# Performance work log

Hardware: AMD Instinct MI355X
Metric: run time of the kernel (lower is better)

The kernel has to match this reference:

```python
import jax, jax.numpy as jnp
import numpy as np

B, T, D, C = 8, 4096, 768, 2048

def setup_inputs() -> dict:
    key = jax.random.key(0)
    k1, k2 = jax.random.split(key)
    embed = jax.random.normal(k1, (B, T, D), dtype=jnp.float32)
    cluster_centers = jax.random.normal(k2, (C, D), dtype=jnp.float32)
    return {"embed": embed, "cluster_centers": cluster_centers}

def reference(embed, cluster_centers):
    x_sq = jnp.sum(embed * embed, axis=-1, keepdims=True)          # (b, t, 1)
    c_sq = jnp.sum(cluster_centers * cluster_centers, axis=-1)     # (c,)
    cross = jnp.einsum('btd,cd->btc', embed, cluster_centers)      # (b, t, c)
    sq_dists = x_sq + c_sq[None, None, :] - 2.0 * cross
    dists = jnp.sqrt(jnp.maximum(sq_dists, 0.0))
    # dists argmax of -cdist == argmin of cdist
    clusters = jnp.argmin(dists, axis=-1)                          # (b, t) int
    return clusters
```

## Files before the change

### kernel.cpp

```cpp
#include <hip/hip_runtime.h>

typedef __fp16 f16x2 __attribute__((ext_vector_type(2)));
typedef __fp16 f16x8 __attribute__((ext_vector_type(8)));
typedef float f32x4 __attribute__((ext_vector_type(4)));

constexpr int MM = 32768;
constexpr int NN = 2048;
constexpr int KK = 768;
constexpr int BM = 128;
constexpr int BN = 128;
constexpr int NKT = KK / 32;
constexpr int NA_UNITS = (MM / 16) * NKT;
constexpr int NB_UNITS = (NN / 16) * NKT;

constexpr size_t WS_APACK = 0;
constexpr size_t WS_BPACK = WS_APACK + (size_t)MM * KK * 4;
constexpr size_t WS_CSQ   = WS_BPACK + (size_t)NN * KK * 4;
constexpr size_t WS_SLOT  = WS_CSQ + (size_t)NN * 4;
constexpr size_t WS_NEED  = WS_SLOT + (size_t)MM * 16 * 8;

__device__ __forceinline__ unsigned bc(f16x2 h) {
    return __builtin_bit_cast(unsigned, h);
}


__global__ __launch_bounds__(256)
void fragpack_kernel(const float* __restrict__ A, const float* __restrict__ Bc,
                     uint4* __restrict__ Ap, uint4* __restrict__ Bp) {
    const int task = blockIdx.x * 4 + (threadIdx.x >> 6);
    const int lane = threadIdx.x & 63;
    const int ln15 = lane & 15;
    const int quad = lane >> 4;

    const bool isB = task >= NA_UNITS;
    const int t = isB ? task - NA_UNITS : task;
    const int tile = t / NKT, kt = t % NKT;
    const float* src = (isB ? Bc : A) + (size_t)(tile * 16 + ln15) * KK + kt * 32 + quad * 8;
    uint4* dst = (isB ? Bp : Ap) + (size_t)t * 128 + lane;

    const float4 v0 = *(const float4*)(src);
    const float4 v1 = *(const float4*)(src + 4);
    f16x2 h0 = __builtin_amdgcn_cvt_pkrtz(v0.x, v0.y);
    f16x2 h1 = __builtin_amdgcn_cvt_pkrtz(v0.z, v0.w);
    f16x2 h2 = __builtin_amdgcn_cvt_pkrtz(v1.x, v1.y);
    f16x2 h3 = __builtin_amdgcn_cvt_pkrtz(v1.z, v1.w);
    f16x2 l0 = __builtin_amdgcn_cvt_pkrtz(v0.x-(float)h0[0], v0.y-(float)h0[1]);
    f16x2 l1 = __builtin_amdgcn_cvt_pkrtz(v0.z-(float)h1[0], v0.w-(float)h1[1]);
    f16x2 l2 = __builtin_amdgcn_cvt_pkrtz(v1.x-(float)h2[0], v1.y-(float)h2[1]);
    f16x2 l3 = __builtin_amdgcn_cvt_pkrtz(v1.z-(float)h3[0], v1.w-(float)h3[1]);
    uint4 hv = {bc(h0), bc(h1), bc(h2), bc(h3)};
    uint4 lv = {bc(l0), bc(l1), bc(l2), bc(l3)};
    dst[0]  = hv;
    dst[64] = lv;
}

__global__ __launch_bounds__(64)
void csq_kernel(const float* __restrict__ cc, float* __restrict__ csq) {
    const int cl = blockIdx.x;
    const int lane = threadIdx.x;
    const float4* row = reinterpret_cast<const float4*>(cc + (size_t)cl * KK);
    float s = 0.f;
#pragma unroll
    for (int w = 0; w < KK / (4 * 64); ++w) {
        float4 v = row[w * 64 + lane];
        s = fmaf(v.x, v.x, s); s = fmaf(v.y, v.y, s);
        s = fmaf(v.z, v.z, s); s = fmaf(v.w, v.w, s);
    }
#pragma unroll
    for (int off = 32; off > 0; off >>= 1) s += __shfl_xor(s, off, 64);
    if (lane == 0) csq[cl] = s;
}

#define MF(a, b, c) __builtin_amdgcn_mfma_f32_16x16x32_f16( \
    __builtin_bit_cast(f16x8, a), __builtin_bit_cast(f16x8, b), c, 0, 0, 0)

__global__ __launch_bounds__(256, 2)
void gemm_pack_kernel(const uint4* __restrict__ Ap, const uint4* __restrict__ Bp,
                      const float* __restrict__ csq, uint2* __restrict__ slots) {
    const int gx = blockIdx.x;
    const int gy = blockIdx.y;
    const int tid  = threadIdx.x;
    const int lane = tid & 63;
    const int ln15 = lane & 15;
    const int quad = lane >> 4;
    const int wave = tid >> 6;
    const int wm = wave >> 1, wn = wave & 1;
    const int tbase = gy * BM;
    const int cb    = gx * BN;

    const uint4* a_ptr[4];
    const uint4* b_ptr[4];
#pragma unroll
    for (int i = 0; i < 4; ++i) {
        a_ptr[i] = Ap + (size_t)(gy * 8 + wm * 4 + i) * NKT * 128 + lane;
        b_ptr[i] = Bp + (size_t)(gx * 8 + wn * 4 + i) * NKT * 128 + lane;
    }

    f32x4 acc[4][4];
#pragma unroll
    for (int i = 0; i < 4; ++i)
#pragma unroll
        for (int j = 0; j < 4; ++j) { f32x4 z = {0.f,0.f,0.f,0.f}; acc[i][j] = z; }

    uint4 Ah0[4], Al0[4], Bh0[4], Bl0[4];
    uint4 Ah1[4], Al1[4], Bh1[4], Bl1[4];

    auto load0 = [&](int kt) {
        const int o = kt * 128;
#pragma unroll
        for (int i = 0; i < 4; ++i) {
            Ah0[i] = a_ptr[i][o]; Al0[i] = a_ptr[i][o + 64];
            Bh0[i] = b_ptr[i][o]; Bl0[i] = b_ptr[i][o + 64];
        }
    };
    auto load1 = [&](int kt) {
        const int o = kt * 128;
#pragma unroll
        for (int i = 0; i < 4; ++i) {
            Ah1[i] = a_ptr[i][o]; Al1[i] = a_ptr[i][o + 64];
            Bh1[i] = b_ptr[i][o]; Bl1[i] = b_ptr[i][o + 64];
        }
    };
    auto comp0 = [&]() {
#pragma unroll
        for (int i = 0; i < 4; ++i)
#pragma unroll
            for (int j = 0; j < 4; ++j) {
                acc[i][j] = MF(Ah0[i], Bh0[j], acc[i][j]);
                acc[i][j] = MF(Ah0[i], Bl0[j], acc[i][j]);
                acc[i][j] = MF(Al0[i], Bh0[j], acc[i][j]);
            }
    };
    auto comp1 = [&]() {
#pragma unroll
        for (int i = 0; i < 4; ++i)
#pragma unroll
            for (int j = 0; j < 4; ++j) {
                acc[i][j] = MF(Ah1[i], Bh1[j], acc[i][j]);
                acc[i][j] = MF(Ah1[i], Bl1[j], acc[i][j]);
                acc[i][j] = MF(Al1[i], Bh1[j], acc[i][j]);
            }
    };

    load0(0);
#pragma unroll 1
    for (int kt = 0; kt < NKT; kt += 2) {
        load1(kt + 1);
        comp0();
        if (kt + 2 < NKT) load0(kt + 2);
        comp1();
    }

    float csq4[4];
#pragma unroll
    for (int j = 0; j < 4; ++j) csq4[j] = csq[cb + wn * 64 + j * 16 + ln15];

    float bval[16]; int bidx[16];
#pragma unroll
    for (int i = 0; i < 4; ++i)
#pragma unroll
        for (int r = 0; r < 4; ++r) {
            const int rid = i * 4 + r;
            float bv_ = csq4[0] - 2.0f * acc[i][0][r];
            int   bi_ = cb + wn * 64 + ln15;
#pragma unroll
            for (int j = 1; j < 4; ++j) {
                const float s = csq4[j] - 2.0f * acc[i][j][r];
                const int   c = cb + wn * 64 + j * 16 + ln15;
                if (s < bv_) { bv_ = s; bi_ = c; }
            }
            bval[rid] = bv_; bidx[rid] = bi_;
        }
#pragma unroll
    for (int off = 1; off < 16; off <<= 1) {
#pragma unroll
        for (int rid = 0; rid < 16; ++rid) {
            const float ov = __shfl_xor(bval[rid], off, 64);
            const int   oi = __shfl_xor(bidx[rid], off, 64);
            if (ov < bval[rid] || (ov == bval[rid] && oi < bidx[rid])) {
                bval[rid] = ov; bidx[rid] = oi;
            }
        }
    }

    __shared__ float vtab[256];
    __shared__ int   itab[256];
    if (ln15 == 0) {
#pragma unroll
        for (int i = 0; i < 4; ++i)
#pragma unroll
            for (int r = 0; r < 4; ++r) {
                const int row = wm * 64 + i * 16 + quad * 4 + r;
                vtab[row * 2 + wn] = bval[i * 4 + r];
                itab[row * 2 + wn] = bidx[i * 4 + r];
            }
    }
    __syncthreads();
    if (tid < 128) {
        float v0 = vtab[tid * 2]; int i0 = itab[tid * 2];
        const float v1 = vtab[tid * 2 + 1]; const int i1 = itab[tid * 2 + 1];
        if (v1 < v0 || (v1 == v0 && i1 < i0)) { v0 = v1; i0 = i1; }
        uint2 e; e.x = __float_as_uint(v0); e.y = (unsigned)i0;
        slots[(size_t)(tbase + tid) * 16 + gx] = e;
    }
}

__global__ __launch_bounds__(256)
void slot_reduce_kernel(const uint2* __restrict__ slots, int* __restrict__ out) {
    const int t = blockIdx.x * 256 + threadIdx.x;
    const uint2* s = slots + (size_t)t * 16;
    float bv = __uint_as_float(s[0].x); int bi = (int)s[0].y;
#pragma unroll
    for (int j = 1; j < 16; ++j) {
        const uint2 e = s[j];
        const float v = __uint_as_float(e.x);
        if (v < bv || (v == bv && (int)e.y < bi)) { bv = v; bi = (int)e.y; }
    }
    out[t] = bi;
}


__global__ __launch_bounds__(256)
void init_ws_kernel(unsigned long long* __restrict__ w) {
    w[blockIdx.x * 256 + threadIdx.x] = 0xFFFFFFFFFFFFFFFFull;
}

__global__ __launch_bounds__(256, 2)
void argmin_mfma_kernel(const float* __restrict__ A, const float* __restrict__ Bc,
                        const float* __restrict__ csq,
                        unsigned long long* __restrict__ ws64) {
    __shared__ unsigned lds[4 * 128 * 20];
    constexpr int AH = 0, AL = 2560, BH = 5120;

    const int tid  = threadIdx.x;
    const int lane = tid & 63;
    const int ln15 = lane & 15;
    const int quad = lane >> 4;
    const int wave = tid >> 6;
    const int wm = wave >> 1, wn = wave & 1;
    const int tbase = blockIdx.x * BM;
    const int cb    = blockIdx.y * BN;

    const int sr  = tid >> 1;
    const int skh = tid & 1;
    const float* gA = A  + (size_t)(tbase + sr) * KK + skh * 16;
    const float* gB = Bc + (size_t)(cb   + sr) * KK + skh * 16;
    const int wword = sr * 20 + skh * 8;

    f32x4 acc[4][4];
#pragma unroll
    for (int i = 0; i < 4; ++i)
#pragma unroll
        for (int j = 0; j < 4; ++j) { f32x4 z = {0.f,0.f,0.f,0.f}; acc[i][j] = z; }

    float4 av[4], bv[4];
#pragma unroll
    for (int p = 0; p < 4; ++p) {
        av[p] = *(const float4*)(gA + p * 4);
        bv[p] = *(const float4*)(gB + p * 4);
    }

    int aw[4], bw[4];
#pragma unroll
    for (int i = 0; i < 4; ++i) {
        aw[i] = AH + (wm * 64 + i * 16 + ln15) * 20 + quad * 4;
        bw[i] = BH + (wn * 64 + i * 16 + ln15) * 20 + quad * 4;
    }

    for (int k0 = 0; k0 < KK; k0 += 32) {
        __syncthreads();
#pragma unroll
        for (int h = 0; h < 2; ++h) {
            float4 v0 = av[2*h], v1 = av[2*h+1];
            f16x2 h00 = __builtin_amdgcn_cvt_pkrtz(v0.x, v0.y);
            f16x2 h01 = __builtin_amdgcn_cvt_pkrtz(v0.z, v0.w);
            f16x2 h10 = __builtin_amdgcn_cvt_pkrtz(v1.x, v1.y);
            f16x2 h11 = __builtin_amdgcn_cvt_pkrtz(v1.z, v1.w);
            f16x2 l00 = __builtin_amdgcn_cvt_pkrtz(v0.x-(float)h00[0], v0.y-(float)h00[1]);
            f16x2 l01 = __builtin_amdgcn_cvt_pkrtz(v0.z-(float)h01[0], v0.w-(float)h01[1]);
            f16x2 l10 = __builtin_amdgcn_cvt_pkrtz(v1.x-(float)h10[0], v1.y-(float)h10[1]);
            f16x2 l11 = __builtin_amdgcn_cvt_pkrtz(v1.z-(float)h11[0], v1.w-(float)h11[1]);
            uint4 hv = {bc(h00), bc(h01), bc(h10), bc(h11)};
            uint4 lv = {bc(l00), bc(l01), bc(l10), bc(l11)};
            *(uint4*)&lds[AH + wword + 4*h] = hv;
            *(uint4*)&lds[AL + wword + 4*h] = lv;

            float4 w0 = bv[2*h], w1 = bv[2*h+1];
            f16x2 g00 = __builtin_amdgcn_cvt_pkrtz(w0.x, w0.y);
            f16x2 g01 = __builtin_amdgcn_cvt_pkrtz(w0.z, w0.w);
            f16x2 g10 = __builtin_amdgcn_cvt_pkrtz(w1.x, w1.y);
            f16x2 g11 = __builtin_amdgcn_cvt_pkrtz(w1.z, w1.w);
            f16x2 m00 = __builtin_amdgcn_cvt_pkrtz(w0.x-(float)g00[0], w0.y-(float)g00[1]);
            f16x2 m01 = __builtin_amdgcn_cvt_pkrtz(w0.z-(float)g01[0], w0.w-(float)g01[1]);
            f16x2 m10 = __builtin_amdgcn_cvt_pkrtz(w1.x-(float)g10[0], w1.y-(float)g10[1]);
            f16x2 m11 = __builtin_amdgcn_cvt_pkrtz(w1.z-(float)g11[0], w1.w-(float)g11[1]);
            uint4 gv = {bc(g00), bc(g01), bc(g10), bc(g11)};
            uint4 mv = {bc(m00), bc(m01), bc(m10), bc(m11)};
            *(uint4*)&lds[BH + wword + 4*h]        = gv;
            *(uint4*)&lds[BH + 2560 + wword + 4*h] = mv;
        }
        __syncthreads();

        const int kn = k0 + 32;
        if (kn < KK) {
#pragma unroll
            for (int p = 0; p < 4; ++p) {
                av[p] = *(const float4*)(gA + kn + p * 4);
                bv[p] = *(const float4*)(gB + kn + p * 4);
            }
        }

        f16x8 a_h[4], a_l[4], b_h[4], b_l[4];
#pragma unroll
        for (int i = 0; i < 4; ++i) {
            a_h[i] = *(const f16x8*)&lds[aw[i]];
            a_l[i] = *(const f16x8*)&lds[aw[i] + 2560];
            b_h[i] = *(const f16x8*)&lds[bw[i]];
            b_l[i] = *(const f16x8*)&lds[bw[i] + 2560];
        }
#pragma unroll
        for (int i = 0; i < 4; ++i)
#pragma unroll
            for (int j = 0; j < 4; ++j) {
                acc[i][j] = __builtin_amdgcn_mfma_f32_16x16x32_f16(a_h[i], b_h[j], acc[i][j], 0, 0, 0);
                acc[i][j] = __builtin_amdgcn_mfma_f32_16x16x32_f16(a_h[i], b_l[j], acc[i][j], 0, 0, 0);
                acc[i][j] = __builtin_amdgcn_mfma_f32_16x16x32_f16(a_l[i], b_h[j], acc[i][j], 0, 0, 0);
            }
    }

    float csq4[4];
#pragma unroll
    for (int j = 0; j < 4; ++j) csq4[j] = csq[cb + wn * 64 + j * 16 + ln15];

    float bval[16]; int bidx[16];
#pragma unroll
    for (int i = 0; i < 4; ++i)
#pragma unroll
        for (int r = 0; r < 4; ++r) {
            const int rid = i * 4 + r;
            float bv_ = csq4[0] - 2.0f * acc[i][0][r];
            int   bi_ = cb + wn * 64 + ln15;
#pragma unroll
            for (int j = 1; j < 4; ++j) {
                const float s = csq4[j] - 2.0f * acc[i][j][r];
                const int   c = cb + wn * 64 + j * 16 + ln15;
                if (s < bv_) { bv_ = s; bi_ = c; }
            }
            bval[rid] = bv_; bidx[rid] = bi_;
        }
#pragma unroll
    for (int off = 1; off < 16; off <<= 1) {
#pragma unroll
        for (int rid = 0; rid < 16; ++rid) {
            const float ov = __shfl_xor(bval[rid], off, 64);
            const int   oi = __shfl_xor(bidx[rid], off, 64);
            if (ov < bval[rid] || (ov == bval[rid] && oi < bidx[rid])) {
                bval[rid] = ov; bidx[rid] = oi;
            }
        }
    }

    __syncthreads();
    float* vtab = (float*)&lds[0];
    int*   itab = (int*)&lds[256];
    if (ln15 == 0) {
#pragma unroll
        for (int i = 0; i < 4; ++i)
#pragma unroll
            for (int r = 0; r < 4; ++r) {
                const int row = wm * 64 + i * 16 + quad * 4 + r;
                vtab[row * 2 + wn] = bval[i * 4 + r];
                itab[row * 2 + wn] = bidx[i * 4 + r];
            }
    }
    __syncthreads();
    if (tid < 128) {
        float v0 = vtab[tid * 2]; int i0 = itab[tid * 2];
        const float v1 = vtab[tid * 2 + 1]; const int i1 = itab[tid * 2 + 1];
        if (v1 < v0 || (v1 == v0 && i1 < i0)) { v0 = v1; i0 = i1; }
        const unsigned b   = __float_as_uint(v0);
        const unsigned key = (b & 0x80000000u) ? ~b : (b | 0x80000000u);
        const unsigned long long pk =
            ((unsigned long long)key << 32) | (unsigned long long)(unsigned)i0;
        atomicMin(&ws64[tbase + tid], pk);
    }
}

__global__ __launch_bounds__(256)
void unpack_kernel(const unsigned long long* __restrict__ w, int* __restrict__ out) {
    const int i = blockIdx.x * 256 + threadIdx.x;
    out[i] = (int)(unsigned)(w[i] & 0xFFFFFFFFull);
}

extern "C" void kernel_launch(void* const* d_in, const int* in_sizes, int n_in,
                              void* d_out, int out_size, void* d_ws, size_t ws_size,
                              hipStream_t stream) {
    const float* embed   = (const float*)d_in[0];
    const float* centers = (const float*)d_in[1];
    int* out = (int*)d_out;

    if (ws_size >= WS_NEED) {
        uint4* Ap = (uint4*)((char*)d_ws + WS_APACK);
        uint4* Bp = (uint4*)((char*)d_ws + WS_BPACK);
        float* csq   = (float*)((char*)d_ws + WS_CSQ);
        uint2* slots = (uint2*)((char*)d_ws + WS_SLOT);
        fragpack_kernel<<<(NA_UNITS + NB_UNITS) / 4, 256, 0, stream>>>(
            embed, centers, Ap, Bp);
        csq_kernel<<<NN, 64, 0, stream>>>(centers, csq);
        gemm_pack_kernel<<<dim3(NN / BN, MM / BM), 256, 0, stream>>>(
            Ap, Bp, csq, slots);
        slot_reduce_kernel<<<MM / 256, 256, 0, stream>>>(slots, out);
    } else {
        unsigned long long* ws64 = (unsigned long long*)d_ws;
        float* csq = (float*)((char*)d_ws + (size_t)MM * 8);
        init_ws_kernel<<<MM / 256, 256, 0, stream>>>(ws64);
        csq_kernel<<<NN, 64, 0, stream>>>(centers, csq);
        argmin_mfma_kernel<<<dim3(MM / BM, NN / BN), 256, 0, stream>>>(
            embed, centers, csq, ws64);
        unpack_kernel<<<MM / 256, 256, 0, stream>>>(ws64, out);
    }
}
```

Baseline: 452.7 us.

## Switch packed GEMM to 32x32x16 MFMA with LDS-staged A tiles

Repacks the fp16 hi/lo fragments for the 32x32x16 MFMA layout and rewrites the main GEMM around that instruction with a 256x128 block tile. The A fragments are staged through shared memory with register prefetch, so the four waves share them instead of each loading from global memory. The epilogue argmin is adapted to the 32-lane reduction. The larger MFMA is meant to raise math density and cut global traffic per FLOP. In exchange it adds barriers per k-step and more accumulator registers (128 floats), which may limit occupancy.

```diff
diff --git a/kernel.cpp b/kernel.cpp
--- a/kernel.cpp
+++ b/kernel.cpp
@@ -2,16 +2,15 @@
 
 typedef __fp16 f16x2 __attribute__((ext_vector_type(2)));
 typedef __fp16 f16x8 __attribute__((ext_vector_type(8)));
+typedef float f32x16 __attribute__((ext_vector_type(16)));
 typedef float f32x4 __attribute__((ext_vector_type(4)));
 
 constexpr int MM = 32768;
 constexpr int NN = 2048;
 constexpr int KK = 768;
-constexpr int BM = 128;
-constexpr int BN = 128;
-constexpr int NKT = KK / 32;
-constexpr int NA_UNITS = (MM / 16) * NKT;
-constexpr int NB_UNITS = (NN / 16) * NKT;
+constexpr int NKT16 = KK / 16;
+constexpr int NA_U = (MM / 32) * NKT16;
+constexpr int NB_U = (NN / 32) * NKT16;
 
 constexpr size_t WS_APACK = 0;
 constexpr size_t WS_BPACK = WS_APACK + (size_t)MM * KK * 4;
@@ -29,13 +28,11 @@
                      uint4* __restrict__ Ap, uint4* __restrict__ Bp) {
     const int task = blockIdx.x * 4 + (threadIdx.x >> 6);
     const int lane = threadIdx.x & 63;
-    const int ln15 = lane & 15;
-    const int quad = lane >> 4;
-
-    const bool isB = task >= NA_UNITS;
-    const int t = isB ? task - NA_UNITS : task;
-    const int tile = t / NKT, kt = t % NKT;
-    const float* src = (isB ? Bc : A) + (size_t)(tile * 16 + ln15) * KK + kt * 32 + quad * 8;
+    const bool isB = task >= NA_U;
+    const int t = isB ? task - NA_U : task;
+    const int tile = t / NKT16, kt = t % NKT16;
+    const float* src = (isB ? Bc : A)
+        + (size_t)(tile * 32 + (lane & 31)) * KK + kt * 16 + (lane >> 5) * 8;
     uint4* dst = (isB ? Bp : Ap) + (size_t)t * 128 + lane;
 
     const float4 v0 = *(const float4*)(src);
@@ -71,175 +68,167 @@
     if (lane == 0) csq[cl] = s;
 }
 
-#define MF(a, b, c) __builtin_amdgcn_mfma_f32_16x16x32_f16( \
+#define MF32(a, b, c) __builtin_amdgcn_mfma_f32_32x32x16_f16( \
     __builtin_bit_cast(f16x8, a), __builtin_bit_cast(f16x8, b), c, 0, 0, 0)
 
 __global__ __launch_bounds__(256, 2)
-void gemm_pack_kernel(const uint4* __restrict__ Ap, const uint4* __restrict__ Bp,
-                      const float* __restrict__ csq, uint2* __restrict__ slots) {
+void gemm32_kernel(const uint4* __restrict__ Ap, const uint4* __restrict__ Bp,
+                   const float* __restrict__ csq, uint2* __restrict__ slots) {
+    __shared__ uint4 lds[2048];
+
     const int gx = blockIdx.x;
     const int gy = blockIdx.y;
+    const int tid  = threadIdx.x;
+    const int lane = tid & 63;
+    const int l31  = lane & 31;
+    const int half = lane >> 5;
+    const int wave = tid >> 6;
+    const int wm = wave >> 1, wn = wave & 1;
+
+    const int c  = tid >> 3, l8 = tid & 7;
+    const int si = c >> 2, spart = (c >> 1) & 1, sks = c & 1;
+    const uint4* aBase = Ap + ((size_t)(gy * 8 + si) * NKT16 + sks) * 128
+                            + spart * 64 + l8;
+    const int ldsW = c * 64 + l8;
+
+    const uint4* bBase[2];
+#pragma unroll
+    for (int j = 0; j < 2; ++j)
+        bBase[j] = Bp + (size_t)(gx * 4 + wn * 2 + j) * NKT16 * 128 + lane;
+
+    f32x16 acc[4][2];
+#pragma unroll
+    for (int i = 0; i < 4; ++i)
+#pragma unroll
+        for (int j = 0; j < 2; ++j)
+#pragma unroll
+            for (int r = 0; r < 16; ++r) acc[i][j][r] = 0.f;
+
+    uint4 st[8];
+#pragma unroll
+    for (int q = 0; q < 8; ++q) st[q] = aBase[q * 8];
+
+#pragma unroll 1
+    for (int kt2 = 0; kt2 < NKT16 / 2; ++kt2) {
+        __syncthreads();
+#pragma unroll
+        for (int q = 0; q < 8; ++q) lds[ldsW + q * 8] = st[q];
+        __syncthreads();
+        if (kt2 + 1 < NKT16 / 2) {
+            const size_t o = (size_t)(kt2 + 1) * 256;
+#pragma unroll
+            for (int q = 0; q < 8; ++q) st[q] = aBase[o + q * 8];
+        }
+        uint4 bfr[2][2][2];
+#pragma unroll
+        for (int ks = 0; ks < 2; ++ks)
+#pragma unroll
+            for (int j = 0; j < 2; ++j) {
+                const int kt = kt2 * 2 + ks;
+                bfr[ks][j][0] = bBase[j][kt * 128];
+                bfr[ks][j][1] = bBase[j][kt * 128 + 64];
+            }
+#pragma unroll
+        for (int ks = 0; ks < 2; ++ks) {
+            uint4 afr[4][2];
+#pragma unroll
+            for (int i = 0; i < 4; ++i) {
+                afr[i][0] = lds[((wm * 4 + i) * 4 + 0 * 2 + ks) * 64 + lane];
+                afr[i][1] = lds[((wm * 4 + i) * 4 + 1 * 2 + ks) * 64 + lane];
+            }
+#pragma unroll
+            for (int i = 0; i < 4; ++i)
+#pragma unroll
+                for (int j = 0; j < 2; ++j)
+                    acc[i][j] = MF32(afr[i][0], bfr[ks][j][0], acc[i][j]);
+#pragma unroll
+            for (int i = 0; i < 4; ++i)
+#pragma unroll
+                for (int j = 0; j < 2; ++j)
+                    acc[i][j] = MF32(afr[i][0], bfr[ks][j][1], acc[i][j]);
+#pragma unroll
+            for (int i = 0; i < 4; ++i)
+#pragma unroll
+                for (int j = 0; j < 2; ++j)
+                    acc[i][j] = MF32(afr[i][1], bfr[ks][j][0], acc[i][j]);
+        }
+    }
+
+    const int cb = gx * 128;
+    float csqv[2];
+#pragma unroll
+    for (int j = 0; j < 2; ++j) csqv[j] = csq[cb + wn * 64 + j * 32 + l31];
+
+    __syncthreads();
+    float* vtab = (float*)&lds[0];
+    int*   itab = (int*)&lds[128];
+#pragma unroll
+    for (int i = 0; i < 4; ++i) {
+#pragma unroll
+        for (int r = 0; r < 16; ++r) {
+            float v0 = csqv[0] - 2.0f * acc[i][0][r];
+            int   i0 = cb + wn * 64 + l31;
+            const float v1 = csqv[1] - 2.0f * acc[i][1][r];
+            const int   i1 = cb + wn * 64 + 32 + l31;
+            if (v1 < v0) { v0 = v1; i0 = i1; }
+#pragma unroll
+            for (int off = 1; off < 32; off <<= 1) {
+                const float ov = __shfl_xor(v0, off, 64);
+                const int   oi = __shfl_xor(i0, off, 64);
+                if (ov < v0 || (ov == v0 && oi < i0)) { v0 = ov; i0 = oi; }
+            }
+            if (l31 == 0) {
+                const int row = wm * 128 + i * 32 + (r & 3) + 8 * (r >> 2) + 4 * half;
+                vtab[row * 2 + wn] = v0;
+                itab[row * 2 + wn] = i0;
+            }
+        }
+    }
+    __syncthreads();
+    {
+        float v0 = vtab[tid * 2]; int i0 = itab[tid * 2];
+        const float v1 = vtab[tid * 2 + 1]; const int i1 = itab[tid * 2 + 1];
+        if (v1 < v0 || (v1 == v0 && i1 < i0)) { v0 = v1; i0 = i1; }
+        uint2 e; e.x = __float_as_uint(v0); e.y = (unsigned)i0;
+        slots[(size_t)(gy * 256 + tid) * 16 + gx] = e;
+    }
+}
+
+__global__ __launch_bounds__(256)
+void slot_reduce_kernel(const uint2* __restrict__ slots, int* __restrict__ out) {
+    const int t = blockIdx.x * 256 + threadIdx.x;
+    const uint2* s = slots + (size_t)t * 16;
+    float bv = __uint_as_float(s[0].x); int bi = (int)s[0].y;
+#pragma unroll
+    for (int j = 1; j < 16; ++j) {
+        const uint2 e = s[j];
+        const float v = __uint_as_float(e.x);
+        if (v < bv || (v == bv && (int)e.y < bi)) { bv = v; bi = (int)e.y; }
+    }
+    out[t] = bi;
+}
+
+
+__global__ __launch_bounds__(256)
+void init_ws_kernel(unsigned long long* __restrict__ w) {
+    w[blockIdx.x * 256 + threadIdx.x] = 0xFFFFFFFFFFFFFFFFull;
+}
+
+__global__ __launch_bounds__(256, 2)
+void argmin_mfma_kernel(const float* __restrict__ A, const float* __restrict__ Bc,
+                        const float* __restrict__ csq,
+                        unsigned long long* __restrict__ ws64) {
+    __shared__ unsigned lds[4 * 128 * 20];
+    constexpr int AH = 0, AL = 2560, BH = 5120;
+
     const int tid  = threadIdx.x;
     const int lane = tid & 63;
     const int ln15 = lane & 15;
     const int quad = lane >> 4;
     const int wave = tid >> 6;
     const int wm = wave >> 1, wn = wave & 1;
-    const int tbase = gy * BM;
-    const int cb    = gx * BN;
-
-    const uint4* a_ptr[4];
-    const uint4* b_ptr[4];
-#pragma unroll
-    for (int i = 0; i < 4; ++i) {
-        a_ptr[i] = Ap + (size_t)(gy * 8 + wm * 4 + i) * NKT * 128 + lane;
-        b_ptr[i] = Bp + (size_t)(gx * 8 + wn * 4 + i) * NKT * 128 + lane;
-    }
-
-    f32x4 acc[4][4];
-#pragma unroll
-    for (int i = 0; i < 4; ++i)
-#pragma unroll
-        for (int j = 0; j < 4; ++j) { f32x4 z = {0.f,0.f,0.f,0.f}; acc[i][j] = z; }
-
-    uint4 Ah0[4], Al0[4], Bh0[4], Bl0[4];
-    uint4 Ah1[4], Al1[4], Bh1[4], Bl1[4];
-
-    auto load0 = [&](int kt) {
-        const int o = kt * 128;
-#pragma unroll
-        for (int i = 0; i < 4; ++i) {
-            Ah0[i] = a_ptr[i][o]; Al0[i] = a_ptr[i][o + 64];
-            Bh0[i] = b_ptr[i][o]; Bl0[i] = b_ptr[i][o + 64];
-        }
-    };
-    auto load1 = [&](int kt) {
-        const int o = kt * 128;
-#pragma unroll
-        for (int i = 0; i < 4; ++i) {
-            Ah1[i] = a_ptr[i][o]; Al1[i] = a_ptr[i][o + 64];
-            Bh1[i] = b_ptr[i][o]; Bl1[i] = b_ptr[i][o + 64];
-        }
-    };
-    auto comp0 = [&]() {
-#pragma unroll
-        for (int i = 0; i < 4; ++i)
-#pragma unroll
-            for (int j = 0; j < 4; ++j) {
-                acc[i][j] = MF(Ah0[i], Bh0[j], acc[i][j]);
-                acc[i][j] = MF(Ah0[i], Bl0[j], acc[i][j]);
-                acc[i][j] = MF(Al0[i], Bh0[j], acc[i][j]);
-            }
-    };
-    auto comp1 = [&]() {
-#pragma unroll
-        for (int i = 0; i < 4; ++i)
-#pragma unroll
-            for (int j = 0; j < 4; ++j) {
-                acc[i][j] = MF(Ah1[i], Bh1[j], acc[i][j]);
-                acc[i][j] = MF(Ah1[i], Bl1[j], acc[i][j]);
-                acc[i][j] = MF(Al1[i], Bh1[j], acc[i][j]);
-            }
-    };
-
-    load0(0);
-#pragma unroll 1
-    for (int kt = 0; kt < NKT; kt += 2) {
-        load1(kt + 1);
-        comp0();
-        if (kt + 2 < NKT) load0(kt + 2);
-        comp1();
-    }
-
-    float csq4[4];
-#pragma unroll
-    for (int j = 0; j < 4; ++j) csq4[j] = csq[cb + wn * 64 + j * 16 + ln15];
-
-    float bval[16]; int bidx[16];
-#pragma unroll
-    for (int i = 0; i < 4; ++i)
-#pragma unroll
-        for (int r = 0; r < 4; ++r) {
-            const int rid = i * 4 + r;
-            float bv_ = csq4[0] - 2.0f * acc[i][0][r];
-            int   bi_ = cb + wn * 64 + ln15;
-#pragma unroll
-            for (int j = 1; j < 4; ++j) {
-                const float s = csq4[j] - 2.0f * acc[i][j][r];
-                const int   c = cb + wn * 64 + j * 16 + ln15;
-                if (s < bv_) { bv_ = s; bi_ = c; }
-            }
-            bval[rid] = bv_; bidx[rid] = bi_;
-        }
-#pragma unroll
-    for (int off = 1; off < 16; off <<= 1) {
-#pragma unroll
-        for (int rid = 0; rid < 16; ++rid) {
-            const float ov = __shfl_xor(bval[rid], off, 64);
-            const int   oi = __shfl_xor(bidx[rid], off, 64);
-            if (ov < bval[rid] || (ov == bval[rid] && oi < bidx[rid])) {
-                bval[rid] = ov; bidx[rid] = oi;
-            }
-        }
-    }
-
-    __shared__ float vtab[256];
-    __shared__ int   itab[256];
-    if (ln15 == 0) {
-#pragma unroll
-        for (int i = 0; i < 4; ++i)
-#pragma unroll
-            for (int r = 0; r < 4; ++r) {
-                const int row = wm * 64 + i * 16 + quad * 4 + r;
-                vtab[row * 2 + wn] = bval[i * 4 + r];
-                itab[row * 2 + wn] = bidx[i * 4 + r];
-            }
-    }
-    __syncthreads();
-    if (tid < 128) {
-        float v0 = vtab[tid * 2]; int i0 = itab[tid * 2];
-        const float v1 = vtab[tid * 2 + 1]; const int i1 = itab[tid * 2 + 1];
-        if (v1 < v0 || (v1 == v0 && i1 < i0)) { v0 = v1; i0 = i1; }
-        uint2 e; e.x = __float_as_uint(v0); e.y = (unsigned)i0;
-        slots[(size_t)(tbase + tid) * 16 + gx] = e;
-    }
-}
-
-__global__ __launch_bounds__(256)
-void slot_reduce_kernel(const uint2* __restrict__ slots, int* __restrict__ out) {
-    const int t = blockIdx.x * 256 + threadIdx.x;
-    const uint2* s = slots + (size_t)t * 16;
-    float bv = __uint_as_float(s[0].x); int bi = (int)s[0].y;
-#pragma unroll
-    for (int j = 1; j < 16; ++j) {
-        const uint2 e = s[j];
-        const float v = __uint_as_float(e.x);
-        if (v < bv || (v == bv && (int)e.y < bi)) { bv = v; bi = (int)e.y; }
-    }
-    out[t] = bi;
-}
-
-
-__global__ __launch_bounds__(256)
-void init_ws_kernel(unsigned long long* __restrict__ w) {
-    w[blockIdx.x * 256 + threadIdx.x] = 0xFFFFFFFFFFFFFFFFull;
-}
-
-__global__ __launch_bounds__(256, 2)
-void argmin_mfma_kernel(const float* __restrict__ A, const float* __restrict__ Bc,
-                        const float* __restrict__ csq,
-                        unsigned long long* __restrict__ ws64) {
-    __shared__ unsigned lds[4 * 128 * 20];
-    constexpr int AH = 0, AL = 2560, BH = 5120;
-
-    const int tid  = threadIdx.x;
-    const int lane = tid & 63;
-    const int ln15 = lane & 15;
-    const int quad = lane >> 4;
-    const int wave = tid >> 6;
-    const int wm = wave >> 1, wn = wave & 1;
-    const int tbase = blockIdx.x * BM;
-    const int cb    = blockIdx.y * BN;
+    const int tbase = blockIdx.x * 128;
+    const int cb    = blockIdx.y * 128;
 
     const int sr  = tid >> 1;
     const int skh = tid & 1;
@@ -343,8 +332,8 @@
 #pragma unroll
             for (int j = 1; j < 4; ++j) {
                 const float s = csq4[j] - 2.0f * acc[i][j][r];
-                const int   c = cb + wn * 64 + j * 16 + ln15;
-                if (s < bv_) { bv_ = s; bi_ = c; }
+                const int   c2 = cb + wn * 64 + j * 16 + ln15;
+                if (s < bv_) { bv_ = s; bi_ = c2; }
             }
             bval[rid] = bv_; bidx[rid] = bi_;
         }
@@ -404,10 +393,10 @@
         uint4* Bp = (uint4*)((char*)d_ws + WS_BPACK);
         float* csq   = (float*)((char*)d_ws + WS_CSQ);
         uint2* slots = (uint2*)((char*)d_ws + WS_SLOT);
-        fragpack_kernel<<<(NA_UNITS + NB_UNITS) / 4, 256, 0, stream>>>(
+        fragpack_kernel<<<(NA_U + NB_U) / 4, 256, 0, stream>>>(
             embed, centers, Ap, Bp);
         csq_kernel<<<NN, 64, 0, stream>>>(centers, csq);
-        gemm_pack_kernel<<<dim3(NN / BN, MM / BM), 256, 0, stream>>>(
+        gemm32_kernel<<<dim3(NN / 128, MM / 256), 256, 0, stream>>>(
             Ap, Bp, csq, slots);
         slot_reduce_kernel<<<MM / 256, 256, 0, stream>>>(slots, out);
     } else {
@@ -415,7 +404,7 @@
         float* csq = (float*)((char*)d_ws + (size_t)MM * 8);
         init_ws_kernel<<<MM / 256, 256, 0, stream>>>(ws64);
         csq_kernel<<<NN, 64, 0, stream>>>(centers, csq);
-        argmin_mfma_kernel<<<dim3(MM / BM, NN / BN), 256, 0, stream>>>(
+        argmin_mfma_kernel<<<dim3(MM / 128, NN / 128), 256, 0, stream>>>(
             embed, centers, csq, ws64);
         unpack_kernel<<<MM / 256, 256, 0, stream>>>(ws64, out);
     }
```

After: 908.2 us. 101% more time.
